# Optimization experiments

Hardware: AMD Instinct MI355X
Metric: run time of the kernel (lower is better)

The kernel has to match this reference:

```python
import jax, jax.numpy as jnp
import numpy as np

B, H, W, C = 8, 64, 64, 256  # N = H*W = 4096, pooled length N//2 = 2048


def setup_inputs() -> dict:
    key = jax.random.key(0)
    k1, k2, k3, k4 = jax.random.split(key, 4)
    scale = np.sqrt(2.0 / C).astype(np.float32)  # he_normal for 1x1 conv
    return {
        "x": jax.random.normal(k1, (B, H, W, C), dtype=jnp.float32),
        "w_theta": jax.random.normal(k2, (C, C), dtype=jnp.float32) * scale,
        "w_phi": jax.random.normal(k3, (C, C), dtype=jnp.float32) * scale,
        "w_g": jax.random.normal(k4, (C, C), dtype=jnp.float32) * scale,
    }


def _maxpool1d(z):
    # MaxPool1D(pool_size=2, strides=2, padding='valid') over axis 1
    b, n, c = z.shape
    return jnp.max(z.reshape(b, n // 2, 2, c), axis=2)


def reference(x, w_theta, w_phi, w_g):
    b, h, w, c = x.shape
    n = h * w
    xf = x.reshape(b, n, c)                       # [B, N, C]
    theta = xf @ w_theta                          # [B, N, C] (1x1 conv)
    phi = _maxpool1d(xf @ w_phi)                  # [B, N//2, C]
    f = jnp.einsum('bnc,bmc->bnm', theta, phi)    # [B, N, N//2] affinity
    f = jax.nn.softmax(f, axis=-1)
    g = _maxpool1d(xf @ w_g)                      # [B, N//2, C]
    y = jnp.einsum('bnm,bmc->bnc', f, g)          # [B, N, C]
    y = y.reshape(b, h, w, c)
    return x + y                                  # residual
```

## Files before the change

kernel.cpp:

```cpp
#include <hip/hip_runtime.h>
#include <stdint.h>

#define CC 256
#define NN 4096
#define MM 2048
#define BB 8
#define NROWS (BB*NN)
#define PROWS (BB*MM)

typedef __attribute__((ext_vector_type(8))) short    short8;
typedef __attribute__((ext_vector_type(8))) _Float16 half8;
typedef __attribute__((ext_vector_type(4))) float    float4v;

__device__ __forceinline__ unsigned short f2bf(float f) {
    unsigned int u = __float_as_uint(f);
    u += 0x7fffu + ((u >> 16) & 1u);
    return (unsigned short)(u >> 16);
}
__device__ __forceinline__ float bf2f(unsigned short h) {
    return __uint_as_float(((unsigned int)h) << 16);
}
__device__ __forceinline__ unsigned short f2h(float f) {
    union { _Float16 h; unsigned short u; } cv; cv.h = (_Float16)f; return cv.u;
}
__device__ __forceinline__ float h2f(unsigned short u) {
    union { _Float16 h; unsigned short u; } cv; cv.u = u; return (float)cv.h;
}

__global__ __launch_bounds__(256) void xsplit_kernel(
    const float* __restrict__ x,
    unsigned short* __restrict__ x_hi,
    unsigned short* __restrict__ x_lo)
{
    const size_t i = ((size_t)blockIdx.x*256 + threadIdx.x) * 8;
    float4v a0 = *(const float4v*)(x + i);
    float4v a1 = *(const float4v*)(x + i + 4);
    short8 h, l;
    #pragma unroll
    for (int j = 0; j < 4; ++j) {
        unsigned short h0 = f2bf(a0[j]);
        h[j]   = (short)h0; l[j]   = (short)f2bf(a0[j] - bf2f(h0));
        unsigned short h1 = f2bf(a1[j]);
        h[4+j] = (short)h1; l[4+j] = (short)f2bf(a1[j] - bf2f(h1));
    }
    *(short8*)(x_hi + i) = h;
    *(short8*)(x_lo + i) = l;
}

__global__ void wsplit_kernel(const float* __restrict__ w_theta,
                              const float* __restrict__ w_phi,
                              const float* __restrict__ w_g,
                              unsigned short* __restrict__ wT_hi,
                              unsigned short* __restrict__ wT_lo)
{
    __shared__ float tile[64][65];
    const int widx = blockIdx.z;
    const int kt = blockIdx.x, ct = blockIdx.y;
    const float* w = (widx == 0) ? w_theta : (widx == 1) ? w_phi : w_g;
    const int t  = threadIdx.x;
    const int tc = t & 63, tr = t >> 6;
    #pragma unroll
    for (int i = 0; i < 16; ++i) {
        const int lk = tr*16 + i;
        tile[lk][tc] = w[(size_t)(kt*64 + lk)*CC + ct*64 + tc];
    }
    __syncthreads();
    #pragma unroll
    for (int i = 0; i < 16; ++i) {
        const int lc = tr*16 + i;
        float v = tile[tc][lc];
        const int c = ct*64 + lc, k = kt*64 + tc;
        unsigned short hh = f2bf(v);
        size_t o = ((size_t)widx*CC + c)*CC + k;
        wT_hi[o] = hh;
        wT_lo[o] = f2bf(v - bf2f(hh));
    }
}

__global__ __launch_bounds__(256, 4) void proj_kernel(
    const unsigned short* __restrict__ x_hi,
    const unsigned short* __restrict__ x_lo,
    const unsigned short* __restrict__ wT_hi,
    const unsigned short* __restrict__ wT_lo,
    unsigned short* __restrict__ th,
    unsigned short* __restrict__ ph,
    unsigned short* __restrict__ g_t)
{
    __shared__ unsigned short wt_hi[64*136];
    __shared__ unsigned short wt_lo[64*136];

    const int tid  = threadIdx.x;
    const int rb   = blockIdx.x & 511;
    const int cv   = blockIdx.x >> 9;
    const int r0   = rb * 64;
    const int widx = cv >> 2;
    const int wc0  = (cv & 3) * 64;
    const unsigned short* wThp = wT_hi + ((size_t)widx*CC + wc0)*CC;
    const unsigned short* wTlp = wT_lo + ((size_t)widx*CC + wc0)*CC;
    const bool split3 = (widx < 2);

    const int wv   = tid >> 6;
    const int lane = tid & 63;
    const int quad = lane >> 4;
    const int l15  = lane & 15;
    const int arow = r0 + wv*16 + l15;
    const unsigned short* axh = x_hi + (size_t)arow*CC + quad*8;
    const unsigned short* axl = x_lo + (size_t)arow*CC + quad*8;

    float4v acc[4];
    #pragma unroll
    for (int nf = 0; nf < 4; ++nf) acc[nf] = (float4v){0.f,0.f,0.f,0.f};

    for (int h = 0; h < 2; ++h) {
        __syncthreads();
        {
            const int j    = tid & 63;
            const int kseg = tid >> 6;
            const size_t base = (size_t)j*CC + h*128 + kseg*32;
            const unsigned short* sh = wThp + base;
            unsigned short* dh = &wt_hi[j*136 + kseg*32];
            #pragma unroll
            for (int u = 0; u < 4; ++u)
                *(uint4*)(dh + u*8) = *(const uint4*)(sh + u*8);
            if (split3) {
                const unsigned short* sl = wTlp + base;
                unsigned short* dl = &wt_lo[j*136 + kseg*32];
                #pragma unroll
                for (int u = 0; u < 4; ++u)
                    *(uint4*)(dl + u*8) = *(const uint4*)(sl + u*8);
            }
        }
        __syncthreads();

        #pragma unroll
        for (int ks = 0; ks < 4; ++ks) {
            short8 a_hi = *(const short8*)(axh + h*128 + ks*32);
            short8 a_lo;
            if (split3) a_lo = *(const short8*)(axl + h*128 + ks*32);
            #pragma unroll
            for (int nf = 0; nf < 4; ++nf) {
                const int wrow = nf*16 + l15;
                short8 b_hi = *(const short8*)&wt_hi[wrow*136 + ks*32 + quad*8];
                acc[nf] = __builtin_amdgcn_mfma_f32_16x16x32_bf16(a_hi, b_hi, acc[nf], 0,0,0);
                if (split3) {
                    short8 b_lo = *(const short8*)&wt_lo[wrow*136 + ks*32 + quad*8];
                    acc[nf] = __builtin_amdgcn_mfma_f32_16x16x32_bf16(a_hi, b_lo, acc[nf], 0,0,0);
                    acc[nf] = __builtin_amdgcn_mfma_f32_16x16x32_bf16(a_lo, b_hi, acc[nf], 0,0,0);
                }
            }
        }
    }

    const int rowbase = r0 + wv*16 + quad*4;
    if (widx == 0) {
        #pragma unroll
        for (int nf = 0; nf < 4; ++nf) {
            const int c = wc0 + nf*16 + l15;
            #pragma unroll
            for (int r = 0; r < 4; ++r)
                th[(size_t)(rowbase + r)*CC + c] = f2h(acc[nf][r]);
        }
    } else if (widx == 1) {
        #pragma unroll
        for (int nf = 0; nf < 4; ++nf) {
            const int c = wc0 + nf*16 + l15;
            #pragma unroll
            for (int rp = 0; rp < 2; ++rp) {
                float v = fmaxf(acc[nf][2*rp], acc[nf][2*rp+1]);
                const int prow = rowbase/2 + rp;
                ph[(size_t)prow*CC + c] = f2h(v);
            }
        }
    } else {
        #pragma unroll
        for (int nf = 0; nf < 4; ++nf) {
            const int c = wc0 + nf*16 + l15;
            #pragma unroll
            for (int rp = 0; rp < 2; ++rp) {
                float v = fmaxf(acc[nf][2*rp], acc[nf][2*rp+1]);
                const int prow = rowbase/2 + rp;
                const int b = prow >> 11;
                const int m = prow & 2047;
                g_t[((size_t)b*CC + c)*MM + m] = f2bf(v);
            }
        }
    }
}

__global__ void phimean_kernel(const unsigned short* __restrict__ ph,
                               float* __restrict__ phbar)
{
    const int b = blockIdx.x >> 6, chunk = blockIdx.x & 63;
    const int c = threadIdx.x;
    const size_t base = ((size_t)b*MM + chunk*32)*CC + c;
    float s = 0.f;
    for (int r = 0; r < 32; ++r) s += h2f(ph[base + (size_t)r*CC]);
    atomicAdd(&phbar[b*CC + c], s * (1.0f/MM));
}

__global__ __launch_bounds__(256, 3) void attn_kernel(
    const float* __restrict__ x,
    const unsigned short* __restrict__ th,
    const unsigned short* __restrict__ ph,
    const unsigned short* __restrict__ g_t,
    const float* __restrict__ phbar,
    float* __restrict__ out)
{
    __shared__ unsigned short s_ph[2][32*264];
    __shared__ unsigned short s_p[2][4][16*40];
    __shared__ float          s_l[64];

    const int tid  = threadIdx.x;
    const int bb   = blockIdx.x & 7;
    const int qt   = blockIdx.x >> 3;
    const int q0   = bb*NN + qt*64;
    const int b    = bb;
    const int wv   = tid >> 6;
    const int lane = tid & 63;
    const int quad = lane >> 4;
    const int l15  = lane & 15;

    const int sti = tid >> 3;
    const int stc = (tid & 7) * 32;
    const size_t phbase = (size_t)b * MM * CC;
    const unsigned short* stsrc = ph + phbase + (size_t)sti*CC + stc;

    half8 t_hi[8];
    {
        const unsigned short* bh = th + (size_t)(q0 + wv*16 + l15)*CC;
        #pragma unroll
        for (int ks = 0; ks < 8; ++ks)
            t_hi[ks] = *(const half8*)(bh + ks*32 + quad*8);
    }

    float sh128[4];
    {
        float sp = 0.f;
        #pragma unroll
        for (int ks = 0; ks < 8; ++ks) {
            const int k0 = ks*32 + quad*8;
            float4v m0 = *(const float4v*)&phbar[b*CC + k0];
            float4v m1 = *(const float4v*)&phbar[b*CC + k0 + 4];
            #pragma unroll
            for (int j = 0; j < 4; ++j) {
                sp += (float)t_hi[ks][j]   * m0[j];
                sp += (float)t_hi[ks][4+j] * m1[j];
            }
        }
        sp += __shfl_xor(sp, 16);
        sp += __shfl_xor(sp, 32);
        #pragma unroll
        for (int r = 0; r < 4; ++r)
            sh128[r] = __shfl(sp, quad*4 + r) + 128.f;
    }

    float4v O[4][4];
    #pragma unroll
    for (int rt = 0; rt < 4; ++rt)
        #pragma unroll
        for (int ct = 0; ct < 4; ++ct) O[rt][ct] = (float4v){0.f,0.f,0.f,0.f};
    float4v accl = (float4v){0.f,0.f,0.f,0.f};

    short8 ones;
    #pragma unroll
    for (int j = 0; j < 8; ++j) ones[j] = (short)0x3F80;

    const unsigned short* gl =
        g_t + ((size_t)b*CC + wv*64 + l15)*MM + quad*8;

    {
        unsigned short* dh = &s_ph[0][sti*264 + stc];
        #pragma unroll
        for (int u = 0; u < 4; ++u)
            *(uint4*)(dh + u*8) = *(const uint4*)(stsrc + u*8);
    }
    __syncthreads();

    for (int kt = 0; kt < 64; ++kt) {
        const int key0 = kt * 32;
        const int cur  = kt & 1;

        uint4 stg[4];
        if (kt < 63) {
            const unsigned short* sn = stsrc + (size_t)(key0 + 32)*CC;
            #pragma unroll
            for (int u = 0; u < 4; ++u) stg[u] = *(const uint4*)(sn + u*8);
        }
        short8 gf[4];
        #pragma unroll
        for (int ct = 0; ct < 4; ++ct)
            gf[ct] = *(const short8*)(gl + (size_t)ct*16*MM + key0);

        float4v S0 = (float4v){0.f,0.f,0.f,0.f};
        float4v S1 = (float4v){0.f,0.f,0.f,0.f};
        #pragma unroll
        for (int ks = 0; ks < 8; ++ks) {
            half8 b0 = *(const half8*)&s_ph[cur][( 0 + l15)*264 + ks*32 + quad*8];
            half8 b1 = *(const half8*)&s_ph[cur][(16 + l15)*264 + ks*32 + quad*8];
            S0 = __builtin_amdgcn_mfma_f32_16x16x32_f16(t_hi[ks], b0, S0, 0,0,0);
            S1 = __builtin_amdgcn_mfma_f32_16x16x32_f16(t_hi[ks], b1, S1, 0,0,0);
        }

        unsigned short* pw = &s_p[cur][wv][0];
        #pragma unroll
        for (int r = 0; r < 4; ++r) {
            float a0 = fminf(fmaxf(S0[r] - sh128[r], -85.f), 85.f);
            float a1 = fminf(fmaxf(S1[r] - sh128[r], -85.f), 85.f);
            pw[(quad*4 + r)*40 + l15]      = f2bf(__expf(a0));
            pw[(quad*4 + r)*40 + 16 + l15] = f2bf(__expf(a1));
        }
        asm volatile("s_waitcnt lgkmcnt(0)" ::: "memory");
        short8 pown = *(const short8*)&s_p[cur][wv][l15*40 + quad*8];
        accl = __builtin_amdgcn_mfma_f32_16x16x32_bf16(pown, ones, accl, 0,0,0);

        if (kt < 63) {
            unsigned short* dh = &s_ph[cur ^ 1][sti*264 + stc];
            #pragma unroll
            for (int u = 0; u < 4; ++u) *(uint4*)(dh + u*8) = stg[u];
        }
        __syncthreads();

        #pragma unroll
        for (int rt = 0; rt < 4; ++rt) {
            short8 pA = *(const short8*)&s_p[cur][rt][l15*40 + quad*8];
            #pragma unroll
            for (int ct = 0; ct < 4; ++ct)
                O[rt][ct] = __builtin_amdgcn_mfma_f32_16x16x32_bf16(pA, gf[ct], O[rt][ct], 0,0,0);
        }
    }

    __syncthreads();
    if (l15 == 0) {
        #pragma unroll
        for (int r = 0; r < 4; ++r) s_l[wv*16 + quad*4 + r] = accl[r];
    }
    __syncthreads();

    #pragma unroll
    for (int rt = 0; rt < 4; ++rt) {
        #pragma unroll
        for (int r = 0; r < 4; ++r) {
            const int row = q0 + rt*16 + quad*4 + r;
            const float rl = 1.0f / s_l[rt*16 + quad*4 + r];
            #pragma unroll
            for (int ct = 0; ct < 4; ++ct) {
                const int c = wv*64 + ct*16 + l15;
                const size_t idx = (size_t)row*CC + c;
                out[idx] = x[idx] + O[rt][ct][r] * rl;
            }
        }
    }
}

extern "C" void kernel_launch(void* const* d_in, const int* in_sizes, int n_in,
                              void* d_out, int out_size, void* d_ws, size_t ws_size,
                              hipStream_t stream) {
    const float* x       = (const float*)d_in[0];
    const float* w_theta = (const float*)d_in[1];
    const float* w_phi   = (const float*)d_in[2];
    const float* w_g     = (const float*)d_in[3];
    float* out = (float*)d_out;

    unsigned short* th    = (unsigned short*)d_ws;
    unsigned short* ph    = th    + (size_t)NROWS*CC;
    unsigned short* g_t   = ph    + (size_t)PROWS*CC;
    unsigned short* x_hi  = g_t   + (size_t)PROWS*CC;
    unsigned short* x_lo  = x_hi  + (size_t)NROWS*CC;
    unsigned short* wT_hi = x_lo  + (size_t)NROWS*CC;
    unsigned short* wT_lo = wT_hi + (size_t)3*CC*CC;
    float*          phbar = (float*)(wT_lo + (size_t)3*CC*CC);

    hipMemsetAsync(phbar, 0, BB*CC*sizeof(float), stream);
    xsplit_kernel<<<NROWS*CC/8/256, 256, 0, stream>>>(x, x_hi, x_lo);
    wsplit_kernel<<<dim3(4,4,3), 256, 0, stream>>>(w_theta, w_phi, w_g, wT_hi, wT_lo);
    proj_kernel<<<6144, 256, 0, stream>>>(x_hi, x_lo, wT_hi, wT_lo, th, ph, g_t);
    phimean_kernel<<<512, 256, 0, stream>>>(ph, phbar);
    attn_kernel<<<NROWS/64, 256, 0, stream>>>(x, th, ph, g_t, phbar, out);
}
```

Before: 286.8 us.

## Warp-specialize attention: score/softmax waves and PV waves pipelined across key tiles

```diff
diff --git a/kernel.cpp b/kernel.cpp
--- a/kernel.cpp
+++ b/kernel.cpp
@@ -198,7 +198,7 @@
     atomicAdd(&phbar[b*CC + c], s * (1.0f/MM));
 }
 
-__global__ __launch_bounds__(256, 3) void attn_kernel(
+__global__ __launch_bounds__(256, 2) void attn_kernel(
     const float* __restrict__ x,
     const unsigned short* __restrict__ th,
     const unsigned short* __restrict__ ph,
@@ -212,8 +212,8 @@
 
     const int tid  = threadIdx.x;
     const int bb   = blockIdx.x & 7;
-    const int qt   = blockIdx.x >> 3;
-    const int q0   = bb*NN + qt*64;
+    const int qtb  = blockIdx.x >> 3;
+    const int q0   = bb*NN + qtb*64;
     const int b    = bb;
     const int wv   = tid >> 6;
     const int lane = tid & 63;
@@ -225,49 +225,6 @@
     const size_t phbase = (size_t)b * MM * CC;
     const unsigned short* stsrc = ph + phbase + (size_t)sti*CC + stc;
 
-    half8 t_hi[8];
-    {
-        const unsigned short* bh = th + (size_t)(q0 + wv*16 + l15)*CC;
-        #pragma unroll
-        for (int ks = 0; ks < 8; ++ks)
-            t_hi[ks] = *(const half8*)(bh + ks*32 + quad*8);
-    }
-
-    float sh128[4];
-    {
-        float sp = 0.f;
-        #pragma unroll
-        for (int ks = 0; ks < 8; ++ks) {
-            const int k0 = ks*32 + quad*8;
-            float4v m0 = *(const float4v*)&phbar[b*CC + k0];
-            float4v m1 = *(const float4v*)&phbar[b*CC + k0 + 4];
-            #pragma unroll
-            for (int j = 0; j < 4; ++j) {
-                sp += (float)t_hi[ks][j]   * m0[j];
-                sp += (float)t_hi[ks][4+j] * m1[j];
-            }
-        }
-        sp += __shfl_xor(sp, 16);
-        sp += __shfl_xor(sp, 32);
-        #pragma unroll
-        for (int r = 0; r < 4; ++r)
-            sh128[r] = __shfl(sp, quad*4 + r) + 128.f;
-    }
-
-    float4v O[4][4];
-    #pragma unroll
-    for (int rt = 0; rt < 4; ++rt)
-        #pragma unroll
-        for (int ct = 0; ct < 4; ++ct) O[rt][ct] = (float4v){0.f,0.f,0.f,0.f};
-    float4v accl = (float4v){0.f,0.f,0.f,0.f};
-
-    short8 ones;
-    #pragma unroll
-    for (int j = 0; j < 8; ++j) ones[j] = (short)0x3F80;
-
-    const unsigned short* gl =
-        g_t + ((size_t)b*CC + wv*64 + l15)*MM + quad*8;
-
     {
         unsigned short* dh = &s_ph[0][sti*264 + stc];
         #pragma unroll
@@ -276,80 +233,190 @@
     }
     __syncthreads();
 
-    for (int kt = 0; kt < 64; ++kt) {
-        const int key0 = kt * 32;
-        const int cur  = kt & 1;
-
-        uint4 stg[4];
-        if (kt < 63) {
-            const unsigned short* sn = stsrc + (size_t)(key0 + 32)*CC;
-            #pragma unroll
-            for (int u = 0; u < 4; ++u) stg[u] = *(const uint4*)(sn + u*8);
-        }
-        short8 gf[4];
-        #pragma unroll
-        for (int ct = 0; ct < 4; ++ct)
-            gf[ct] = *(const short8*)(gl + (size_t)ct*16*MM + key0);
-
-        float4v S0 = (float4v){0.f,0.f,0.f,0.f};
-        float4v S1 = (float4v){0.f,0.f,0.f,0.f};
-        #pragma unroll
-        for (int ks = 0; ks < 8; ++ks) {
-            half8 b0 = *(const half8*)&s_ph[cur][( 0 + l15)*264 + ks*32 + quad*8];
-            half8 b1 = *(const half8*)&s_ph[cur][(16 + l15)*264 + ks*32 + quad*8];
-            S0 = __builtin_amdgcn_mfma_f32_16x16x32_f16(t_hi[ks], b0, S0, 0,0,0);
-            S1 = __builtin_amdgcn_mfma_f32_16x16x32_f16(t_hi[ks], b1, S1, 0,0,0);
-        }
-
-        unsigned short* pw = &s_p[cur][wv][0];
-        #pragma unroll
-        for (int r = 0; r < 4; ++r) {
-            float a0 = fminf(fmaxf(S0[r] - sh128[r], -85.f), 85.f);
-            float a1 = fminf(fmaxf(S1[r] - sh128[r], -85.f), 85.f);
-            pw[(quad*4 + r)*40 + l15]      = f2bf(__expf(a0));
-            pw[(quad*4 + r)*40 + 16 + l15] = f2bf(__expf(a1));
-        }
-        asm volatile("s_waitcnt lgkmcnt(0)" ::: "memory");
-        short8 pown = *(const short8*)&s_p[cur][wv][l15*40 + quad*8];
-        accl = __builtin_amdgcn_mfma_f32_16x16x32_bf16(pown, ones, accl, 0,0,0);
-
-        if (kt < 63) {
-            unsigned short* dh = &s_ph[cur ^ 1][sti*264 + stc];
-            #pragma unroll
-            for (int u = 0; u < 4; ++u) *(uint4*)(dh + u*8) = stg[u];
-        }
+    if (wv < 2) {
+        half8 t0[8], t1[8];
+        {
+            const unsigned short* bh0 = th + (size_t)(q0 + (wv*2+0)*16 + l15)*CC;
+            const unsigned short* bh1 = th + (size_t)(q0 + (wv*2+1)*16 + l15)*CC;
+            #pragma unroll
+            for (int ks = 0; ks < 8; ++ks) {
+                t0[ks] = *(const half8*)(bh0 + ks*32 + quad*8);
+                t1[ks] = *(const half8*)(bh1 + ks*32 + quad*8);
+            }
+        }
+        float sh0[4], sh1[4];
+        #pragma unroll
+        for (int qt = 0; qt < 2; ++qt) {
+            float sp = 0.f;
+            #pragma unroll
+            for (int ks = 0; ks < 8; ++ks) {
+                const int k0 = ks*32 + quad*8;
+                float4v m0 = *(const float4v*)&phbar[b*CC + k0];
+                float4v m1 = *(const float4v*)&phbar[b*CC + k0 + 4];
+                half8 tv = qt ? t1[ks] : t0[ks];
+                #pragma unroll
+                for (int j = 0; j < 4; ++j) {
+                    sp += (float)tv[j]   * m0[j];
+                    sp += (float)tv[4+j] * m1[j];
+                }
+            }
+            sp += __shfl_xor(sp, 16);
+            sp += __shfl_xor(sp, 32);
+            #pragma unroll
+            for (int r = 0; r < 4; ++r) {
+                float v = __shfl(sp, quad*4 + r) + 128.f;
+                if (qt) sh1[r] = v; else sh0[r] = v;
+            }
+        }
+
+        float4v accl0 = (float4v){0.f,0.f,0.f,0.f};
+        float4v accl1 = (float4v){0.f,0.f,0.f,0.f};
+        short8 ones;
+        #pragma unroll
+        for (int j = 0; j < 8; ++j) ones[j] = (short)0x3F80;
+
+        for (int kt = 0; kt < 64; ++kt) {
+            const int key0 = kt * 32;
+            const int cur  = kt & 1;
+
+            uint4 stg[4];
+            if (kt < 63) {
+                const unsigned short* sn = stsrc + (size_t)(key0 + 32)*CC;
+                #pragma unroll
+                for (int u = 0; u < 4; ++u) stg[u] = *(const uint4*)(sn + u*8);
+            }
+
+            float4v S00 = (float4v){0.f,0.f,0.f,0.f};
+            float4v S01 = (float4v){0.f,0.f,0.f,0.f};
+            float4v S10 = (float4v){0.f,0.f,0.f,0.f};
+            float4v S11 = (float4v){0.f,0.f,0.f,0.f};
+            #pragma unroll
+            for (int ks = 0; ks < 8; ++ks) {
+                half8 b0 = *(const half8*)&s_ph[cur][( 0 + l15)*264 + ks*32 + quad*8];
+                half8 b1 = *(const half8*)&s_ph[cur][(16 + l15)*264 + ks*32 + quad*8];
+                S00 = __builtin_amdgcn_mfma_f32_16x16x32_f16(t0[ks], b0, S00, 0,0,0);
+                S01 = __builtin_amdgcn_mfma_f32_16x16x32_f16(t0[ks], b1, S01, 0,0,0);
+                S10 = __builtin_amdgcn_mfma_f32_16x16x32_f16(t1[ks], b0, S10, 0,0,0);
+                S11 = __builtin_amdgcn_mfma_f32_16x16x32_f16(t1[ks], b1, S11, 0,0,0);
+            }
+
+            {
+                unsigned short* pw0 = &s_p[cur][wv*2+0][0];
+                unsigned short* pw1 = &s_p[cur][wv*2+1][0];
+                #pragma unroll
+                for (int r = 0; r < 4; ++r) {
+                    float a0 = fminf(fmaxf(S00[r] - sh0[r], -85.f), 85.f);
+                    float a1 = fminf(fmaxf(S01[r] - sh0[r], -85.f), 85.f);
+                    pw0[(quad*4 + r)*40 + l15]      = f2bf(__expf(a0));
+                    pw0[(quad*4 + r)*40 + 16 + l15] = f2bf(__expf(a1));
+                    float a2 = fminf(fmaxf(S10[r] - sh1[r], -85.f), 85.f);
+                    float a3 = fminf(fmaxf(S11[r] - sh1[r], -85.f), 85.f);
+                    pw1[(quad*4 + r)*40 + l15]      = f2bf(__expf(a2));
+                    pw1[(quad*4 + r)*40 + 16 + l15] = f2bf(__expf(a3));
+                }
+            }
+            asm volatile("s_waitcnt lgkmcnt(0)" ::: "memory");
+            {
+                short8 p0 = *(const short8*)&s_p[cur][wv*2+0][l15*40 + quad*8];
+                accl0 = __builtin_amdgcn_mfma_f32_16x16x32_bf16(p0, ones, accl0, 0,0,0);
+                short8 p1 = *(const short8*)&s_p[cur][wv*2+1][l15*40 + quad*8];
+                accl1 = __builtin_amdgcn_mfma_f32_16x16x32_bf16(p1, ones, accl1, 0,0,0);
+            }
+            if (kt < 63) {
+                unsigned short* dh = &s_ph[cur ^ 1][sti*264 + stc];
+                #pragma unroll
+                for (int u = 0; u < 4; ++u) *(uint4*)(dh + u*8) = stg[u];
+            }
+            __syncthreads();
+        }
+
+        if (l15 == 0) {
+            #pragma unroll
+            for (int r = 0; r < 4; ++r) {
+                s_l[(wv*2+0)*16 + quad*4 + r] = accl0[r];
+                s_l[(wv*2+1)*16 + quad*4 + r] = accl1[r];
+            }
+        }
+    } else {
+        const int cw = wv - 2;
+        const unsigned short* gl =
+            g_t + ((size_t)b*CC + cw*128 + l15)*MM + quad*8;
+
+        float4v O[4][8];
+        #pragma unroll
+        for (int qt = 0; qt < 4; ++qt)
+            #pragma unroll
+            for (int ct = 0; ct < 8; ++ct) O[qt][ct] = (float4v){0.f,0.f,0.f,0.f};
+
+        for (int kt = 0; kt < 64; ++kt) {
+            const int cur = kt & 1;
+
+            uint4 stg[4];
+            if (kt < 63) {
+                const unsigned short* sn = stsrc + (size_t)(kt*32 + 32)*CC;
+                #pragma unroll
+                for (int u = 0; u < 4; ++u) stg[u] = *(const uint4*)(sn + u*8);
+            }
+
+            if (kt > 0) {
+                const int key0 = (kt-1) * 32;
+                const int pb   = (kt-1) & 1;
+                short8 gf[8];
+                #pragma unroll
+                for (int ct = 0; ct < 8; ++ct)
+                    gf[ct] = *(const short8*)(gl + (size_t)ct*16*MM + key0);
+                #pragma unroll
+                for (int qt = 0; qt < 4; ++qt) {
+                    short8 pA = *(const short8*)&s_p[pb][qt][l15*40 + quad*8];
+                    #pragma unroll
+                    for (int ct = 0; ct < 8; ++ct)
+                        O[qt][ct] = __builtin_amdgcn_mfma_f32_16x16x32_bf16(pA, gf[ct], O[qt][ct], 0,0,0);
+                }
+            }
+
+            if (kt < 63) {
+                unsigned short* dh = &s_ph[cur ^ 1][sti*264 + stc];
+                #pragma unroll
+                for (int u = 0; u < 4; ++u) *(uint4*)(dh + u*8) = stg[u];
+            }
+            __syncthreads();
+        }
+
+        {
+            const int key0 = 63 * 32;
+            short8 gf[8];
+            #pragma unroll
+            for (int ct = 0; ct < 8; ++ct)
+                gf[ct] = *(const short8*)(gl + (size_t)ct*16*MM + key0);
+            #pragma unroll
+            for (int qt = 0; qt < 4; ++qt) {
+                short8 pA = *(const short8*)&s_p[1][qt][l15*40 + quad*8];
+                #pragma unroll
+                for (int ct = 0; ct < 8; ++ct)
+                    O[qt][ct] = __builtin_amdgcn_mfma_f32_16x16x32_bf16(pA, gf[ct], O[qt][ct], 0,0,0);
+            }
+        }
+
         __syncthreads();
 
         #pragma unroll
-        for (int rt = 0; rt < 4; ++rt) {
-            short8 pA = *(const short8*)&s_p[cur][rt][l15*40 + quad*8];
-            #pragma unroll
-            for (int ct = 0; ct < 4; ++ct)
-                O[rt][ct] = __builtin_amdgcn_mfma_f32_16x16x32_bf16(pA, gf[ct], O[rt][ct], 0,0,0);
-        }
+        for (int qt = 0; qt < 4; ++qt) {
+            #pragma unroll
+            for (int r = 0; r < 4; ++r) {
+                const int row = q0 + qt*16 + quad*4 + r;
+                const float rl = 1.0f / s_l[qt*16 + quad*4 + r];
+                #pragma unroll
+                for (int ct = 0; ct < 8; ++ct) {
+                    const int c = cw*128 + ct*16 + l15;
+                    const size_t idx = (size_t)row*CC + c;
+                    out[idx] = x[idx] + O[qt][ct][r] * rl;
+                }
+            }
+        }
+        return;
     }
 
     __syncthreads();
-    if (l15 == 0) {
-        #pragma unroll
-        for (int r = 0; r < 4; ++r) s_l[wv*16 + quad*4 + r] = accl[r];
-    }
-    __syncthreads();
-
-    #pragma unroll
-    for (int rt = 0; rt < 4; ++rt) {
-        #pragma unroll
-        for (int r = 0; r < 4; ++r) {
-            const int row = q0 + rt*16 + quad*4 + r;
-            const float rl = 1.0f / s_l[rt*16 + quad*4 + r];
-            #pragma unroll
-            for (int ct = 0; ct < 4; ++ct) {
-                const int c = wv*64 + ct*16 + l15;
-                const size_t idx = (size_t)row*CC + c;
-                out[idx] = x[idx] + O[rt][ct][r] * rl;
-            }
-        }
-    }
 }
 
 extern "C" void kernel_launch(void* const* d_in, const int* in_sizes, int n_in,
```

Result: slower. 322.5 us (+12.5%).
